# Kernel optimization log

Hardware: AMD Instinct MI355X
Metric: run time of the kernel (lower is better)

The kernel has to match this reference:

```python
import jax, jax.numpy as jnp
import numpy as np

B = 1024        # probe batch
Q = 65536       # queue_size (number of identities in momentum queue)
D = 512         # feat_dim
MARGIN = 0.4
SCALE = 32.0
HARD_NEG = 10   # min(max(int(Q*0.0002), 3), 10)


def setup_inputs() -> dict:
    key = jax.random.key(0)
    k1, k2, k3, k4 = jax.random.split(key, 4)
    p = jax.random.normal(k1, (B, D), dtype=jnp.float32)
    p = p / jnp.linalg.norm(p, axis=1, keepdims=True)
    queue = jax.random.uniform(k2, (2, Q, D), dtype=jnp.float32)
    queue = queue / jnp.linalg.norm(queue, axis=2, keepdims=True)  # F.normalize(queue, dim=2)
    label = jax.random.randint(k3, (B,), 0, Q)
    label = jnp.where(jnp.arange(B) % 4 == 0, -1, label)
    # binary mask buffer marking queue slots whose second copy is active
    mask = (jax.random.uniform(k4, (Q, 1)) < 0.1).astype(jnp.float32)
    return {"p": p, "queue": queue, "mask": mask, "label": label}


def _add_margin_am(cos_theta, label):
    # cos_theta: [B, Q], label: [B] with -1 marking outliers
    pos_mask = label != -1                                  # [B]
    safe_label = jnp.where(pos_mask, label, 0)
    onehot = jax.nn.one_hot(safe_label, cos_theta.shape[1], dtype=cos_theta.dtype)
    # AM-softmax: subtract margin at the ground-truth logit, then scale + CE
    logits = (cos_theta - MARGIN * onehot) * SCALE          # [B, Q]
    log_z = jax.nn.logsumexp(logits, axis=1)                # [B]
    gt = jnp.take_along_axis(cos_theta, safe_label[:, None], axis=1)[:, 0]
    ce = log_z - (gt - MARGIN) * SCALE                      # per-row cross entropy
    n_pos = jnp.sum(pos_mask)
    cls_loss = jnp.where(
        n_pos > 0,
        jnp.sum(jnp.where(pos_mask, ce, 0.0)) / jnp.maximum(n_pos, 1),
        0.0,
    )
    # hard-negative mining over outlier rows: top-k (replaces torch argsort+gather)
    top_vals, _ = jax.lax.top_k(cos_theta, HARD_NEG)        # [B, HARD_NEG]
    hard = jnp.clip(top_vals, 0.0)
    neg_per_row = jnp.mean(hard, axis=1)                    # [B]
    n_neg = jnp.sum(~pos_mask)
    neg_loss = jnp.where(
        n_neg > 0,
        jnp.sum(jnp.where(~pos_mask, neg_per_row, 0.0)) / jnp.maximum(n_neg, 1),
        0.0,
    )
    return cls_loss + neg_loss


def reference(p, queue, mask, label):
    # cos_theta1 = F.linear(p, queue[0])
    cos1 = jnp.einsum('bd,qd->bq', p, queue[0])
    # weight = mask * queue[1] + (1 - mask) * queue[0]  (computed under no_grad in torch)
    weight = mask * queue[1] + (1.0 - mask) * queue[0]
    cos2 = jnp.einsum('bd,qd->bq', p, weight)
    loss = _add_margin_am(cos1, label) + _add_margin_am(cos2, label)
    return loss
```

## Files before the change

### kernel.cpp

```cpp
#include <hip/hip_runtime.h>
#include <stdint.h>

#define B_ 1024
#define Q_ 65536
#define D_ 512
#define MT 128
#define NT 128
#define BK 64
#define NSPLIT 64
#define NCHUNK (Q_ / NSPLIT)
#define NTILES (NCHUNK / NT)
#define KITERS (D_ / BK)

#define SCALE32 32.0f
#define C32 46.16624130844683f

#define WS_ACC  0
#define WS_LSE  4096
#define WS_TOPK (1u * 1024u * 1024u)
#define WS_PBF  (8u * 1024u * 1024u)
#define WS_QBF0 (12u * 1024u * 1024u)
#define WS_WBF  (76u * 1024u * 1024u)

#define SA_OFF 0
#define SB0_OFF 16384
#define SB1_OFF 32768

typedef __attribute__((ext_vector_type(8))) short short8;
typedef __attribute__((ext_vector_type(4))) short short4v;
typedef __attribute__((ext_vector_type(4))) float f32x4;

__device__ __forceinline__ unsigned short f2bf(float x) {
  union { float f; uint32_t u; } v; v.f = x;
  uint32_t r = v.u + 0x7fffu + ((v.u >> 16) & 1u);
  return (unsigned short)(r >> 16);
}

__device__ __forceinline__ float bf2f(short u) {
  union { uint32_t i; float f; } v;
  v.i = ((uint32_t)(unsigned short)u) << 16;
  return v.f;
}

__device__ __forceinline__ void async16(void* lds, const void* g) {
  void* gg = (void*)g;
  __builtin_amdgcn_global_load_lds(
      (__attribute__((address_space(1))) unsigned int*)gg,
      (__attribute__((address_space(3))) unsigned int*)lds,
      16, 0, 0);
}

__device__ __forceinline__ void tkins(float v,
    float& t0, float& t1, float& t2, float& t3, float& t4,
    float& t5, float& t6, float& t7, float& t8, float& t9) {
  if (v > t9) {
    t9 = (v > t8) ? t8 : v;
    t8 = (v > t8) ? ((v > t7) ? t7 : v) : t8;
    t7 = (v > t7) ? ((v > t6) ? t6 : v) : t7;
    t6 = (v > t6) ? ((v > t5) ? t5 : v) : t6;
    t5 = (v > t5) ? ((v > t4) ? t4 : v) : t5;
    t4 = (v > t4) ? ((v > t3) ? t3 : v) : t4;
    t3 = (v > t3) ? ((v > t2) ? t2 : v) : t3;
    t2 = (v > t2) ? ((v > t1) ? t1 : v) : t2;
    t1 = (v > t1) ? ((v > t0) ? t0 : v) : t1;
    t0 = (v > t0) ? v : t0;
  }
}

#define TKA(v, a) tkins((v), a[0], a[1], a[2], a[3], a[4], a[5], a[6], a[7], a[8], a[9])

__global__ void cvt_all(const float* __restrict__ q, const float* __restrict__ p,
                        const float* __restrict__ mask,
                        unsigned short* __restrict__ qbf0,
                        unsigned short* __restrict__ wbf,
                        unsigned short* __restrict__ pbf) {
  const int wv = threadIdx.x >> 6;
  const int lane = threadIdx.x & 63;
  const int b = blockIdx.x;
  if (b < Q_ / 4) {
    const int row = b * 4 + wv;
    const float* q0r = q + (size_t)row * D_ + lane * 8;
    float4 a = ((const float4*)q0r)[0];
    float4 bb = ((const float4*)q0r)[1];
    short8 o;
    o[0] = (short)f2bf(a.x); o[1] = (short)f2bf(a.y);
    o[2] = (short)f2bf(a.z); o[3] = (short)f2bf(a.w);
    o[4] = (short)f2bf(bb.x); o[5] = (short)f2bf(bb.y);
    o[6] = (short)f2bf(bb.z); o[7] = (short)f2bf(bb.w);
    *(short8*)(qbf0 + (size_t)row * D_ + lane * 8) = o;
    float m = mask[row];
    if (m != 0.0f) {
      const float* q1r = q0r + (size_t)Q_ * D_;
      float4 c = ((const float4*)q1r)[0];
      float4 d = ((const float4*)q1r)[1];
      a.x = fmaf(m, c.x - a.x, a.x); a.y = fmaf(m, c.y - a.y, a.y);
      a.z = fmaf(m, c.z - a.z, a.z); a.w = fmaf(m, c.w - a.w, a.w);
      bb.x = fmaf(m, d.x - bb.x, bb.x); bb.y = fmaf(m, d.y - bb.y, bb.y);
      bb.z = fmaf(m, d.z - bb.z, bb.z); bb.w = fmaf(m, d.w - bb.w, bb.w);
      o[0] = (short)f2bf(a.x); o[1] = (short)f2bf(a.y);
      o[2] = (short)f2bf(a.z); o[3] = (short)f2bf(a.w);
      o[4] = (short)f2bf(bb.x); o[5] = (short)f2bf(bb.y);
      o[6] = (short)f2bf(bb.z); o[7] = (short)f2bf(bb.w);
      *(short8*)(wbf + (size_t)row * D_ + lane * 8) = o;
    }
  } else {
    const int row = (b - Q_ / 4) * 4 + wv;
    const float* pr = p + (size_t)row * D_ + lane * 8;
    float4 a = ((const float4*)pr)[0];
    float4 bb = ((const float4*)pr)[1];
    short8 o;
    o[0] = (short)f2bf(a.x); o[1] = (short)f2bf(a.y);
    o[2] = (short)f2bf(a.z); o[3] = (short)f2bf(a.w);
    o[4] = (short)f2bf(bb.x); o[5] = (short)f2bf(bb.y);
    o[6] = (short)f2bf(bb.z); o[7] = (short)f2bf(bb.w);
    *(short8*)(pbf + (size_t)row * D_ + lane * 8) = o;
  }
}

__global__ __launch_bounds__(256, 2) void fused_gemm_partial(
    const unsigned short* __restrict__ pbf,
    const unsigned short* __restrict__ qbf0,
    const unsigned short* __restrict__ wbf,
    const float* __restrict__ maskp,
    const int* __restrict__ label,
    char* __restrict__ ws) {
  __shared__ __align__(16) unsigned char smem[49152];
  __shared__ float maskb[NT];
  __shared__ float zacc[MT][4];
  __shared__ int olist[MT];
  __shared__ int rowmap[MT];
  __shared__ int sh_ocount;

  const int tid = threadIdx.x;
  const int split = blockIdx.x;
  const int mblk = blockIdx.y;
  const int lane = tid & 63;
  const int wv = tid >> 6;
  const int wr = wv >> 1;
  const int wc = wv & 1;
  const int lr = lane & 15;
  const int lg = lane >> 4;

  if (tid == 0) sh_ocount = 0;
  if (tid < MT) {
    rowmap[tid] = -1;
    zacc[tid][0] = 0.0f; zacc[tid][1] = 0.0f;
    zacc[tid][2] = 0.0f; zacc[tid][3] = 0.0f;
  }
  __syncthreads();
  if (tid < MT) {
    if (label[mblk * MT + tid] == -1) {
      int k = atomicAdd(&sh_ocount, 1);
      olist[k] = tid;
    }
  }
  __syncthreads();
  const int noc = sh_ocount;
  if (tid < noc) rowmap[olist[tid]] = tid;
  __syncthreads();
  const int nchunks = (noc + 31) >> 5;

  const int srow = lane >> 3;
  const int sc16 = (lane & 7) ^ srow;
  const size_t g_lane_off = (size_t)srow * D_ + sc16 * 8;

  float T[10];
#pragma unroll
  for (int i = 0; i < 10; ++i) T[i] = -1e30f;

  for (int nt = 0; nt < NTILES; ++nt) {
    const int nbase = split * NCHUNK + nt * NT;
    if (tid < NT) maskb[tid] = maskp[nbase + tid];
    __syncthreads();

    const unsigned short* b1b[4];
#pragma unroll
    for (int t = 0; t < 4; ++t) {
      const int rowl = (wv * 4 + t) * 8 + srow;
      b1b[t] = (maskb[rowl] != 0.0f) ? wbf : qbf0;
    }

    f32x4 acc0[4][4], acc1[4][4];
#pragma unroll
    for (int i = 0; i < 4; ++i)
#pragma unroll
      for (int j = 0; j < 4; ++j) {
        f32x4 z = {0.0f, 0.0f, 0.0f, 0.0f};
        acc0[i][j] = z;
        acc1[i][j] = z;
      }

    for (int kk = 0; kk < KITERS; ++kk) {
      const size_t kcol = (size_t)kk * BK;
#pragma unroll
      for (int t = 0; t < 4; ++t) {
        const int slot = wv * 4 + t;
        const size_t rbase = (size_t)slot * 8;
        async16(smem + SA_OFF + slot * 1024,
                pbf + ((size_t)mblk * MT + rbase) * D_ + kcol + g_lane_off);
        async16(smem + SB0_OFF + slot * 1024,
                qbf0 + ((size_t)nbase + rbase) * D_ + kcol + g_lane_off);
        async16(smem + SB1_OFF + slot * 1024,
                b1b[t] + ((size_t)nbase + rbase) * D_ + kcol + g_lane_off);
      }
      __syncthreads();

#pragma unroll
      for (int s = 0; s < 2; ++s) {
        const int xs = ((s * 4 + lg) ^ (lr & 7)) * 16;
        short8 af[4], bf[4];
#pragma unroll
        for (int i = 0; i < 4; ++i)
          af[i] = *(const short8*)(smem + SA_OFF + (wr * 64 + i * 16 + lr) * 128 + xs);
#pragma unroll
        for (int j = 0; j < 4; ++j)
          bf[j] = *(const short8*)(smem + SB0_OFF + (wc * 64 + j * 16 + lr) * 128 + xs);
#pragma unroll
        for (int i = 0; i < 4; ++i)
#pragma unroll
          for (int j = 0; j < 4; ++j)
            acc0[i][j] = __builtin_amdgcn_mfma_f32_16x16x32_bf16(af[i], bf[j], acc0[i][j], 0, 0, 0);
#pragma unroll
        for (int j = 0; j < 4; ++j)
          bf[j] = *(const short8*)(smem + SB1_OFF + (wc * 64 + j * 16 + lr) * 128 + xs);
#pragma unroll
        for (int i = 0; i < 4; ++i)
#pragma unroll
          for (int j = 0; j < 4; ++j)
            acc1[i][j] = __builtin_amdgcn_mfma_f32_16x16x32_bf16(af[i], bf[j], acc1[i][j], 0, 0, 0);
      }
      __syncthreads();
    }

#pragma unroll
    for (int i = 0; i < 4; ++i)
#pragma unroll
      for (int k = 0; k < 4; ++k) {
        float a0 = 0.0f, a1 = 0.0f;
#pragma unroll
        for (int j = 0; j < 4; ++j) {
          a0 += __builtin_amdgcn_exp2f(fmaf(acc0[i][j][k], C32, -C32));
          a1 += __builtin_amdgcn_exp2f(fmaf(acc1[i][j][k], C32, -C32));
        }
#pragma unroll
        for (int m = 1; m < 16; m <<= 1) {
          a0 += __shfl_xor(a0, m, 64);
          a1 += __shfl_xor(a1, m, 64);
        }
        if (lr == 0) {
          const int r = wr * 64 + i * 16 + lg * 4 + k;
          zacc[r][wc * 2 + 0] += a0;
          zacc[r][wc * 2 + 1] += a1;
        }
      }

    for (int c = 0; c < nchunks; ++c) {
      unsigned short* cp = (unsigned short*)smem;
#pragma unroll
      for (int i = 0; i < 4; ++i)
#pragma unroll
        for (int k = 0; k < 4; ++k) {
          const int r = wr * 64 + i * 16 + lg * 4 + k;
          const int o = rowmap[r];
          const int ol = o - c * 32;
          if (o >= 0 && ol >= 0 && ol < 32) {
#pragma unroll
            for (int j = 0; j < 4; ++j) {
              const int col = wc * 64 + j * 16 + lr;
              cp[ol * 128 + col] = f2bf(acc0[i][j][k]);
              cp[(32 + ol) * 128 + col] = f2bf(acc1[i][j][k]);
            }
          }
        }
      __syncthreads();

      {
        float tl[10];
#pragma unroll
        for (int r = 0; r < 10; ++r) tl[r] = -1e30f;
        const int pair = tid >> 2;
        const int q4 = tid & 3;
        const int orow = pair >> 1, mat = pair & 1;
        const int o = c * 32 + orow;
        if (o < noc) {
          const unsigned short* rp = cp + (mat * 32 + orow) * 128 + q4 * 32;
#pragma unroll
          for (int cc = 0; cc < 8; ++cc) {
            short4v v = *(const short4v*)(rp + cc * 4);
            TKA(bf2f(v.x), tl); TKA(bf2f(v.y), tl);
            TKA(bf2f(v.z), tl); TKA(bf2f(v.w), tl);
          }
          float ot[10];
#pragma unroll
          for (int r = 0; r < 10; ++r) ot[r] = __shfl_xor(tl[r], 1, 64);
#pragma unroll
          for (int r = 0; r < 10; ++r) TKA(ot[r], tl);
#pragma unroll
          for (int r = 0; r < 10; ++r) ot[r] = __shfl_xor(tl[r], 2, 64);
#pragma unroll
          for (int r = 0; r < 10; ++r) TKA(ot[r], tl);
          if (q4 == 0) {
            if (c == 0) {
#pragma unroll
              for (int r = 0; r < 10; ++r) TKA(tl[r], T);
            } else {
              float* slot = (float*)(ws + WS_TOPK) +
                  ((size_t)(mat * B_ + mblk * MT + olist[o]) * NSPLIT + split) * 10;
              if (nt == 0) {
#pragma unroll
                for (int r = 0; r < 10; ++r) slot[r] = tl[r];
              } else {
                float cur[10];
#pragma unroll
                for (int r = 0; r < 10; ++r) cur[r] = slot[r];
#pragma unroll
                for (int r = 0; r < 10; ++r) TKA(tl[r], cur);
#pragma unroll
                for (int r = 0; r < 10; ++r) slot[r] = cur[r];
              }
            }
          }
        }
      }
      __syncthreads();
    }
  }

  if (tid < MT) {
    float2* lseo = (float2*)(ws + WS_LSE);
    lseo[(size_t)(mblk * MT + tid) * NSPLIT + split] =
        make_float2(zacc[tid][0] + zacc[tid][2], zacc[tid][1] + zacc[tid][3]);
  }
  {
    const int pair = tid >> 2;
    const int q4 = tid & 3;
    const int orow = pair >> 1, mat = pair & 1;
    if (q4 == 0 && orow < noc && orow < 32) {
      float* slot = (float*)(ws + WS_TOPK) +
          ((size_t)(mat * B_ + mblk * MT + olist[orow]) * NSPLIT + split) * 10;
#pragma unroll
      for (int r = 0; r < 10; ++r) slot[r] = T[r];
    }
  }
}

__global__ void finalize_rows(
    const float* __restrict__ p, const float* __restrict__ queue,
    const float* __restrict__ maskp, const int* __restrict__ label,
    char* __restrict__ ws, float* __restrict__ out) {
  const int row = blockIdx.x;
  const int l = threadIdx.x >> 6;
  const int lane = threadIdx.x & 63;
  const int lab = label[row];
  float* wsf = (float*)ws;
  int* wsi = (int*)ws;

  if (lab != -1) {
    const float2* lsep = (const float2*)(ws + WS_LSE) + (size_t)row * NSPLIT;
    float2 zz = lsep[lane];
    float z = (l == 0) ? zz.x : zz.y;
#pragma unroll
    for (int o = 1; o < 64; o <<= 1) z += __shfl_xor(z, o, 64);

    const float* prow = p + (size_t)row * D_;
    const float* q0r = queue + (size_t)lab * D_;
    const float* q1r = queue + ((size_t)Q_ + (size_t)lab) * D_;
    int c = lane * 8;
    float4 a0 = *(const float4*)(prow + c);
    float4 a1 = *(const float4*)(prow + c + 4);
    float4 b0 = *(const float4*)(q0r + c);
    float4 b1 = *(const float4*)(q0r + c + 4);
    float d0 = a0.x * b0.x + a0.y * b0.y + a0.z * b0.z + a0.w * b0.w
             + a1.x * b1.x + a1.y * b1.y + a1.z * b1.z + a1.w * b1.w;
    float d1 = 0.0f;
    if (l == 1) {
      float4 c0 = *(const float4*)(q1r + c);
      float4 c1 = *(const float4*)(q1r + c + 4);
      d1 = a0.x * c0.x + a0.y * c0.y + a0.z * c0.z + a0.w * c0.w
         + a1.x * c1.x + a1.y * c1.y + a1.z * c1.z + a1.w * c1.w;
    }
#pragma unroll
    for (int o = 1; o < 64; o <<= 1) {
      d0 += __shfl_xor(d0, o, 64);
      d1 += __shfl_xor(d1, o, 64);
    }
    float gt;
    if (l == 0) gt = d0;
    else { float m = maskp[lab]; gt = fmaf(m, d1 - d0, d0); }

    if (lane == 0) {
      float e1 = __builtin_amdgcn_exp2f(fmaf(gt, C32, -C32));
      float e2 = __builtin_amdgcn_exp2f(fmaf(gt - 0.4f, C32, -C32));
      float Zc = z - e1 + e2;
      float ce = 32.0f + __logf(Zc) - (gt - 0.4f) * SCALE32;
      atomicAdd(&wsf[0], ce);
      if (l == 0) atomicAdd(&wsi[2], 1);
    }
  } else {
    const float* tp = (const float*)(ws + WS_TOPK) +
                      ((size_t)l * B_ + row) * NSPLIT * 10 + (size_t)lane * 10;
    float t0 = tp[0], t1 = tp[1], t2 = tp[2], t3 = tp[3], t4 = tp[4];
    float t5 = tp[5], t6 = tp[6], t7 = tp[7], t8 = tp[8], t9 = tp[9];
    float ssum = 0.0f;
#pragma unroll
    for (int r10 = 0; r10 < 10; ++r10) {
      float v = t0;
      int idx = lane;
#pragma unroll
      for (int o = 1; o < 64; o <<= 1) {
        float ov = __shfl_xor(v, o, 64);
        int oi = __shfl_xor(idx, o, 64);
        bool take = (ov > v) || (ov == v && oi < idx);
        v = take ? ov : v;
        idx = take ? oi : idx;
      }
      ssum += fmaxf(v, 0.0f);
      if (idx == lane) {
        t0 = t1; t1 = t2; t2 = t3; t3 = t4; t4 = t5;
        t5 = t6; t6 = t7; t7 = t8; t8 = t9; t9 = -1e30f;
      }
    }
    if (lane == 0) {
      atomicAdd(&wsf[1], ssum * 0.1f);
      if (l == 0) atomicAdd(&wsi[3], 1);
    }
  }

  __syncthreads();
  if (threadIdx.x == 0) {
    __threadfence();
    int old = atomicAdd(&wsi[4], 1);
    if (old == B_ - 1) {
      float ce = atomicAdd(&wsf[0], 0.0f);
      float ng = atomicAdd(&wsf[1], 0.0f);
      int np = atomicAdd(&wsi[2], 0);
      int nn = atomicAdd(&wsi[3], 0);
      float loss = 0.0f;
      if (np > 0) loss += ce / (float)np;
      if (nn > 0) loss += ng / (float)nn;
      out[0] = loss;
    }
  }
}

extern "C" void kernel_launch(void* const* d_in, const int* in_sizes, int n_in,
                              void* d_out, int out_size, void* d_ws, size_t ws_size,
                              hipStream_t stream) {
  const float* p     = (const float*)d_in[0];
  const float* queue = (const float*)d_in[1];
  const float* maskp = (const float*)d_in[2];
  const int*   label = (const int*)d_in[3];
  float* out = (float*)d_out;
  char* ws = (char*)d_ws;

  unsigned short* pbf  = (unsigned short*)(ws + WS_PBF);
  unsigned short* qbf0 = (unsigned short*)(ws + WS_QBF0);
  unsigned short* wbf  = (unsigned short*)(ws + WS_WBF);

  hipMemsetAsync(ws, 0, 32, stream);

  cvt_all<<<Q_ / 4 + B_ / 4, 256, 0, stream>>>(queue, p, maskp, qbf0, wbf, pbf);

  dim3 g1(NSPLIT, B_ / MT);
  fused_gemm_partial<<<g1, 256, 0, stream>>>(pbf, qbf0, wbf, maskp, label, ws);
  finalize_rows<<<B_, 128, 0, stream>>>(p, queue, maskp, label, ws, out);
}
```

Measured before the change: 594.9 us.

## Compute second GEMM only on masked rows via compacted delta correction

The second matrix product differed from the first only on the roughly 10% of queue rows whose mask is set. So the main GEMM now computes one product, and a separate compacted GEMM over masked rows (their q0 and blended copies) gives a log-sum-exp delta and top-k candidates for the second loss. Top-k for the shared product marks masked columns as -inf and merges them with the compacted results. This roughly halves MFMA work and B-tile traffic, at the cost of an atomic compaction pass, an extra memset, a fixed cap of MMAX masked rows, and a higher split count and occupancy target.

```diff
diff --git a/kernel.cpp b/kernel.cpp
--- a/kernel.cpp
+++ b/kernel.cpp
@@ -7,24 +7,28 @@
 #define MT 128
 #define NT 128
 #define BK 64
-#define NSPLIT 64
+#define NSPLIT 128
 #define NCHUNK (Q_ / NSPLIT)
 #define NTILES (NCHUNK / NT)
 #define KITERS (D_ / BK)
+#define MMAX 8192
+#define MTILES (MMAX / NT)
 
 #define SCALE32 32.0f
 #define C32 46.16624130844683f
 
-#define WS_ACC  0
-#define WS_LSE  4096
-#define WS_TOPK (1u * 1024u * 1024u)
-#define WS_PBF  (8u * 1024u * 1024u)
-#define WS_QBF0 (12u * 1024u * 1024u)
-#define WS_WBF  (76u * 1024u * 1024u)
+#define WS_ZDELTA 64
+#define WS_LSE    8192
+#define WS_TOPK   (1u << 20)
+#define WS_TOPKM  (6u << 20)
+#define WS_PBF    (12u << 20)
+#define WS_QBF0   (16u << 20)
+#define WS_QMC    (80u << 20)
+#define WS_WMC    (88u << 20)
 
 #define SA_OFF 0
-#define SB0_OFF 16384
-#define SB1_OFF 32768
+#define SB_OFF 16384
+#define CPSTRIDE 136
 
 typedef __attribute__((ext_vector_type(8))) short short8;
 typedef __attribute__((ext_vector_type(4))) short short4v;
@@ -66,14 +70,15 @@
     t0 = (v > t0) ? v : t0;
   }
 }
-
 #define TKA(v, a) tkins((v), a[0], a[1], a[2], a[3], a[4], a[5], a[6], a[7], a[8], a[9])
 
 __global__ void cvt_all(const float* __restrict__ q, const float* __restrict__ p,
                         const float* __restrict__ mask,
                         unsigned short* __restrict__ qbf0,
-                        unsigned short* __restrict__ wbf,
-                        unsigned short* __restrict__ pbf) {
+                        unsigned short* __restrict__ pbf,
+                        unsigned short* __restrict__ qmc,
+                        unsigned short* __restrict__ wmc,
+                        int* __restrict__ wsi) {
   const int wv = threadIdx.x >> 6;
   const int lane = threadIdx.x & 63;
   const int b = blockIdx.x;
@@ -90,18 +95,26 @@
     *(short8*)(qbf0 + (size_t)row * D_ + lane * 8) = o;
     float m = mask[row];
     if (m != 0.0f) {
+      int idx = 0;
+      if (lane == 0) idx = atomicAdd(&wsi[5], 1);
+      idx = __shfl(idx, 0, 64);
       const float* q1r = q0r + (size_t)Q_ * D_;
       float4 c = ((const float4*)q1r)[0];
       float4 d = ((const float4*)q1r)[1];
-      a.x = fmaf(m, c.x - a.x, a.x); a.y = fmaf(m, c.y - a.y, a.y);
-      a.z = fmaf(m, c.z - a.z, a.z); a.w = fmaf(m, c.w - a.w, a.w);
-      bb.x = fmaf(m, d.x - bb.x, bb.x); bb.y = fmaf(m, d.y - bb.y, bb.y);
-      bb.z = fmaf(m, d.z - bb.z, bb.z); bb.w = fmaf(m, d.w - bb.w, bb.w);
-      o[0] = (short)f2bf(a.x); o[1] = (short)f2bf(a.y);
-      o[2] = (short)f2bf(a.z); o[3] = (short)f2bf(a.w);
-      o[4] = (short)f2bf(bb.x); o[5] = (short)f2bf(bb.y);
-      o[6] = (short)f2bf(bb.z); o[7] = (short)f2bf(bb.w);
-      *(short8*)(wbf + (size_t)row * D_ + lane * 8) = o;
+      float4 wa, wb;
+      wa.x = fmaf(m, c.x - a.x, a.x); wa.y = fmaf(m, c.y - a.y, a.y);
+      wa.z = fmaf(m, c.z - a.z, a.z); wa.w = fmaf(m, c.w - a.w, a.w);
+      wb.x = fmaf(m, d.x - bb.x, bb.x); wb.y = fmaf(m, d.y - bb.y, bb.y);
+      wb.z = fmaf(m, d.z - bb.z, bb.z); wb.w = fmaf(m, d.w - bb.w, bb.w);
+      short8 o2;
+      o2[0] = (short)f2bf(wa.x); o2[1] = (short)f2bf(wa.y);
+      o2[2] = (short)f2bf(wa.z); o2[3] = (short)f2bf(wa.w);
+      o2[4] = (short)f2bf(wb.x); o2[5] = (short)f2bf(wb.y);
+      o2[6] = (short)f2bf(wb.z); o2[7] = (short)f2bf(wb.w);
+      if (idx < MMAX) {
+        *(short8*)(qmc + (size_t)idx * D_ + lane * 8) = o;
+        *(short8*)(wmc + (size_t)idx * D_ + lane * 8) = o2;
+      }
     }
   } else {
     const int row = (b - Q_ / 4) * 4 + wv;
@@ -117,16 +130,16 @@
   }
 }
 
-__global__ __launch_bounds__(256, 2) void fused_gemm_partial(
+__global__ __launch_bounds__(256, 3) void main_gemm(
     const unsigned short* __restrict__ pbf,
     const unsigned short* __restrict__ qbf0,
-    const unsigned short* __restrict__ wbf,
     const float* __restrict__ maskp,
     const int* __restrict__ label,
     char* __restrict__ ws) {
-  __shared__ __align__(16) unsigned char smem[49152];
+  __shared__ __align__(16) unsigned char smem[32768];
+  __shared__ float Tlds[256][11];
   __shared__ float maskb[NT];
-  __shared__ float zacc[MT][4];
+  __shared__ float zacc[MT][2];
   __shared__ int olist[MT];
   __shared__ int rowmap[MT];
   __shared__ int sh_ocount;
@@ -145,8 +158,9 @@
   if (tid < MT) {
     rowmap[tid] = -1;
     zacc[tid][0] = 0.0f; zacc[tid][1] = 0.0f;
-    zacc[tid][2] = 0.0f; zacc[tid][3] = 0.0f;
-  }
+  }
+#pragma unroll
+  for (int i = 0; i < 10; ++i) Tlds[tid][i] = -1e30f;
   __syncthreads();
   if (tid < MT) {
     if (label[mblk * MT + tid] == -1) {
@@ -164,30 +178,18 @@
   const int sc16 = (lane & 7) ^ srow;
   const size_t g_lane_off = (size_t)srow * D_ + sc16 * 8;
 
-  float T[10];
-#pragma unroll
-  for (int i = 0; i < 10; ++i) T[i] = -1e30f;
-
   for (int nt = 0; nt < NTILES; ++nt) {
     const int nbase = split * NCHUNK + nt * NT;
     if (tid < NT) maskb[tid] = maskp[nbase + tid];
     __syncthreads();
 
-    const unsigned short* b1b[4];
-#pragma unroll
-    for (int t = 0; t < 4; ++t) {
-      const int rowl = (wv * 4 + t) * 8 + srow;
-      b1b[t] = (maskb[rowl] != 0.0f) ? wbf : qbf0;
-    }
-
-    f32x4 acc0[4][4], acc1[4][4];
+    f32x4 acc[4][4];
 #pragma unroll
     for (int i = 0; i < 4; ++i)
 #pragma unroll
       for (int j = 0; j < 4; ++j) {
         f32x4 z = {0.0f, 0.0f, 0.0f, 0.0f};
-        acc0[i][j] = z;
-        acc1[i][j] = z;
+        acc[i][j] = z;
       }
 
     for (int kk = 0; kk < KITERS; ++kk) {
@@ -198,13 +200,10 @@
         const size_t rbase = (size_t)slot * 8;
         async16(smem + SA_OFF + slot * 1024,
                 pbf + ((size_t)mblk * MT + rbase) * D_ + kcol + g_lane_off);
-        async16(smem + SB0_OFF + slot * 1024,
+        async16(smem + SB_OFF + slot * 1024,
                 qbf0 + ((size_t)nbase + rbase) * D_ + kcol + g_lane_off);
-        async16(smem + SB1_OFF + slot * 1024,
-                b1b[t] + ((size_t)nbase + rbase) * D_ + kcol + g_lane_off);
       }
       __syncthreads();
-
 #pragma unroll
       for (int s = 0; s < 2; ++s) {
         const int xs = ((s * 4 + lg) ^ (lr & 7)) * 16;
@@ -214,43 +213,29 @@
           af[i] = *(const short8*)(smem + SA_OFF + (wr * 64 + i * 16 + lr) * 128 + xs);
 #pragma unroll
         for (int j = 0; j < 4; ++j)
-          bf[j] = *(const short8*)(smem + SB0_OFF + (wc * 64 + j * 16 + lr) * 128 + xs);
+          bf[j] = *(const short8*)(smem + SB_OFF + (wc * 64 + j * 16 + lr) * 128 + xs);
 #pragma unroll
         for (int i = 0; i < 4; ++i)
 #pragma unroll
           for (int j = 0; j < 4; ++j)
-            acc0[i][j] = __builtin_amdgcn_mfma_f32_16x16x32_bf16(af[i], bf[j], acc0[i][j], 0, 0, 0);
+            acc[i][j] = __builtin_amdgcn_mfma_f32_16x16x32_bf16(af[i], bf[j], acc[i][j], 0, 0, 0);
+      }
+      __syncthreads();
+    }
+
+#pragma unroll
+    for (int i = 0; i < 4; ++i)
+#pragma unroll
+      for (int k = 0; k < 4; ++k) {
+        float a0 = 0.0f;
 #pragma unroll
         for (int j = 0; j < 4; ++j)
-          bf[j] = *(const short8*)(smem + SB1_OFF + (wc * 64 + j * 16 + lr) * 128 + xs);
-#pragma unroll
-        for (int i = 0; i < 4; ++i)
-#pragma unroll
-          for (int j = 0; j < 4; ++j)
-            acc1[i][j] = __builtin_amdgcn_mfma_f32_16x16x32_bf16(af[i], bf[j], acc1[i][j], 0, 0, 0);
-      }
-      __syncthreads();
-    }
-
-#pragma unroll
-    for (int i = 0; i < 4; ++i)
-#pragma unroll
-      for (int k = 0; k < 4; ++k) {
-        float a0 = 0.0f, a1 = 0.0f;
-#pragma unroll
-        for (int j = 0; j < 4; ++j) {
-          a0 += __builtin_amdgcn_exp2f(fmaf(acc0[i][j][k], C32, -C32));
-          a1 += __builtin_amdgcn_exp2f(fmaf(acc1[i][j][k], C32, -C32));
-        }
-#pragma unroll
-        for (int m = 1; m < 16; m <<= 1) {
-          a0 += __shfl_xor(a0, m, 64);
-          a1 += __shfl_xor(a1, m, 64);
-        }
+          a0 += __builtin_amdgcn_exp2f(fmaf(acc[i][j][k], C32, -C32));
+#pragma unroll
+        for (int m = 1; m < 16; m <<= 1) a0 += __shfl_xor(a0, m, 64);
         if (lr == 0) {
           const int r = wr * 64 + i * 16 + lg * 4 + k;
-          zacc[r][wc * 2 + 0] += a0;
-          zacc[r][wc * 2 + 1] += a1;
+          zacc[r][wc] += a0;
         }
       }
 
@@ -267,80 +252,267 @@
 #pragma unroll
             for (int j = 0; j < 4; ++j) {
               const int col = wc * 64 + j * 16 + lr;
-              cp[ol * 128 + col] = f2bf(acc0[i][j][k]);
-              cp[(32 + ol) * 128 + col] = f2bf(acc1[i][j][k]);
+              unsigned short v = (maskb[col] != 0.0f) ? (unsigned short)0xFF80
+                                                      : f2bf(acc[i][j][k]);
+              cp[ol * CPSTRIDE + col] = v;
             }
           }
         }
       __syncthreads();
 
-      {
-        float tl[10];
-#pragma unroll
-        for (int r = 0; r < 10; ++r) tl[r] = -1e30f;
-        const int pair = tid >> 2;
-        const int q4 = tid & 3;
-        const int orow = pair >> 1, mat = pair & 1;
-        const int o = c * 32 + orow;
+      const int orow = tid >> 3;
+      const int q8 = tid & 7;
+      const int o = c * 32 + orow;
+      if (c == 0) {
         if (o < noc) {
-          const unsigned short* rp = cp + (mat * 32 + orow) * 128 + q4 * 32;
-#pragma unroll
-          for (int cc = 0; cc < 8; ++cc) {
+          float tl[10];
+#pragma unroll
+          for (int r = 0; r < 10; ++r) tl[r] = Tlds[tid][r];
+          const unsigned short* rp = cp + orow * CPSTRIDE + q8 * 16;
+#pragma unroll
+          for (int cc = 0; cc < 4; ++cc) {
             short4v v = *(const short4v*)(rp + cc * 4);
             TKA(bf2f(v.x), tl); TKA(bf2f(v.y), tl);
             TKA(bf2f(v.z), tl); TKA(bf2f(v.w), tl);
           }
-          float ot[10];
-#pragma unroll
-          for (int r = 0; r < 10; ++r) ot[r] = __shfl_xor(tl[r], 1, 64);
-#pragma unroll
-          for (int r = 0; r < 10; ++r) TKA(ot[r], tl);
-#pragma unroll
-          for (int r = 0; r < 10; ++r) ot[r] = __shfl_xor(tl[r], 2, 64);
-#pragma unroll
-          for (int r = 0; r < 10; ++r) TKA(ot[r], tl);
-          if (q4 == 0) {
-            if (c == 0) {
-#pragma unroll
-              for (int r = 0; r < 10; ++r) TKA(tl[r], T);
-            } else {
-              float* slot = (float*)(ws + WS_TOPK) +
-                  ((size_t)(mat * B_ + mblk * MT + olist[o]) * NSPLIT + split) * 10;
-              if (nt == 0) {
-#pragma unroll
-                for (int r = 0; r < 10; ++r) slot[r] = tl[r];
-              } else {
-                float cur[10];
-#pragma unroll
-                for (int r = 0; r < 10; ++r) cur[r] = slot[r];
-#pragma unroll
-                for (int r = 0; r < 10; ++r) TKA(tl[r], cur);
-#pragma unroll
-                for (int r = 0; r < 10; ++r) slot[r] = cur[r];
-              }
-            }
+#pragma unroll
+          for (int r = 0; r < 10; ++r) Tlds[tid][r] = tl[r];
+        }
+      } else {
+        float tl[10];
+#pragma unroll
+        for (int r = 0; r < 10; ++r) tl[r] = -1e30f;
+        if (o < noc) {
+          const unsigned short* rp = cp + orow * CPSTRIDE + q8 * 16;
+#pragma unroll
+          for (int cc = 0; cc < 4; ++cc) {
+            short4v v = *(const short4v*)(rp + cc * 4);
+            TKA(bf2f(v.x), tl); TKA(bf2f(v.y), tl);
+            TKA(bf2f(v.z), tl); TKA(bf2f(v.w), tl);
           }
         }
+        float ot[10];
+#pragma unroll
+        for (int m = 1; m < 8; m <<= 1) {
+#pragma unroll
+          for (int r = 0; r < 10; ++r) ot[r] = __shfl_xor(tl[r], m, 64);
+#pragma unroll
+          for (int r = 0; r < 10; ++r) TKA(ot[r], tl);
+        }
+        if (q8 == 0 && o < noc) {
+          float* slot = (float*)(ws + WS_TOPK) +
+              ((size_t)(mblk * MT + olist[o]) * NSPLIT + split) * 10;
+          if (nt == 0) {
+#pragma unroll
+            for (int r = 0; r < 10; ++r) slot[r] = tl[r];
+          } else {
+            float cur[10];
+#pragma unroll
+            for (int r = 0; r < 10; ++r) cur[r] = slot[r];
+#pragma unroll
+            for (int r = 0; r < 10; ++r) TKA(tl[r], cur);
+#pragma unroll
+            for (int r = 0; r < 10; ++r) slot[r] = cur[r];
+          }
+        }
       }
       __syncthreads();
     }
   }
 
   if (tid < MT) {
-    float2* lseo = (float2*)(ws + WS_LSE);
-    lseo[(size_t)(mblk * MT + tid) * NSPLIT + split] =
-        make_float2(zacc[tid][0] + zacc[tid][2], zacc[tid][1] + zacc[tid][3]);
+    ((float*)(ws + WS_LSE))[(size_t)(mblk * MT + tid) * NSPLIT + split] =
+        zacc[tid][0] + zacc[tid][1];
   }
   {
-    const int pair = tid >> 2;
-    const int q4 = tid & 3;
-    const int orow = pair >> 1, mat = pair & 1;
-    if (q4 == 0 && orow < noc && orow < 32) {
+    const int orow = tid >> 3;
+    const int q8 = tid & 7;
+    float tl[10], ot[10];
+#pragma unroll
+    for (int r = 0; r < 10; ++r) tl[r] = Tlds[tid][r];
+#pragma unroll
+    for (int m = 1; m < 8; m <<= 1) {
+#pragma unroll
+      for (int r = 0; r < 10; ++r) ot[r] = __shfl_xor(tl[r], m, 64);
+#pragma unroll
+      for (int r = 0; r < 10; ++r) TKA(ot[r], tl);
+    }
+    if (q8 == 0 && orow < noc) {
       float* slot = (float*)(ws + WS_TOPK) +
-          ((size_t)(mat * B_ + mblk * MT + olist[orow]) * NSPLIT + split) * 10;
-#pragma unroll
-      for (int r = 0; r < 10; ++r) slot[r] = T[r];
-    }
+          ((size_t)(mblk * MT + olist[orow]) * NSPLIT + split) * 10;
+#pragma unroll
+      for (int r = 0; r < 10; ++r) slot[r] = tl[r];
+    }
+  }
+}
+
+__global__ __launch_bounds__(256, 3) void masked_gemm(
+    const unsigned short* __restrict__ pbf,
+    const unsigned short* __restrict__ qmc,
+    const unsigned short* __restrict__ wmc,
+    const int* __restrict__ label,
+    char* __restrict__ ws) {
+  __shared__ __align__(16) unsigned char smem[32768];
+  __shared__ float zacc[MT][2];
+  __shared__ int olist[MT];
+  __shared__ int rowmap[MT];
+  __shared__ int sh_ocount;
+
+  const int tid = threadIdx.x;
+  const int tile = blockIdx.x;
+  const int mblk = blockIdx.y;
+  const int half = blockIdx.z;
+  const int lane = tid & 63;
+  const int wv = tid >> 6;
+  const int wr = wv >> 1;
+  const int wc = wv & 1;
+  const int lr = lane & 15;
+  const int lg = lane >> 4;
+  const int* wsi = (const int*)ws;
+
+  if (tid == 0) sh_ocount = 0;
+  if (tid < MT) {
+    rowmap[tid] = -1;
+    zacc[tid][0] = 0.0f; zacc[tid][1] = 0.0f;
+  }
+  __syncthreads();
+  if (tid < MT) {
+    if (label[mblk * MT + tid] == -1) {
+      int k = atomicAdd(&sh_ocount, 1);
+      olist[k] = tid;
+    }
+  }
+  __syncthreads();
+  const int noc = sh_ocount;
+  if (tid < noc) rowmap[olist[tid]] = tid;
+  __syncthreads();
+  const int nchunks = (noc + 31) >> 5;
+  const int mcnt = wsi[5];
+
+  if (tile * NT >= mcnt) {
+    if (tid < noc) {
+      float* slot = (float*)(ws + WS_TOPKM) +
+          (((size_t)half * B_ + mblk * MT + olist[tid]) * MTILES + tile) * 10;
+#pragma unroll
+      for (int r = 0; r < 10; ++r) slot[r] = -1e30f;
+    }
+    return;
+  }
+
+  const unsigned short* bsrc = half ? wmc : qmc;
+  const int nbase = tile * NT;
+  const int srow = lane >> 3;
+  const int sc16 = (lane & 7) ^ srow;
+  const size_t g_lane_off = (size_t)srow * D_ + sc16 * 8;
+
+  f32x4 acc[4][4];
+#pragma unroll
+  for (int i = 0; i < 4; ++i)
+#pragma unroll
+    for (int j = 0; j < 4; ++j) {
+      f32x4 z = {0.0f, 0.0f, 0.0f, 0.0f};
+      acc[i][j] = z;
+    }
+
+  for (int kk = 0; kk < KITERS; ++kk) {
+    const size_t kcol = (size_t)kk * BK;
+#pragma unroll
+    for (int t = 0; t < 4; ++t) {
+      const int slot = wv * 4 + t;
+      const size_t rbase = (size_t)slot * 8;
+      async16(smem + SA_OFF + slot * 1024,
+              pbf + ((size_t)mblk * MT + rbase) * D_ + kcol + g_lane_off);
+      async16(smem + SB_OFF + slot * 1024,
+              bsrc + ((size_t)nbase + rbase) * D_ + kcol + g_lane_off);
+    }
+    __syncthreads();
+#pragma unroll
+    for (int s = 0; s < 2; ++s) {
+      const int xs = ((s * 4 + lg) ^ (lr & 7)) * 16;
+      short8 af[4], bf[4];
+#pragma unroll
+      for (int i = 0; i < 4; ++i)
+        af[i] = *(const short8*)(smem + SA_OFF + (wr * 64 + i * 16 + lr) * 128 + xs);
+#pragma unroll
+      for (int j = 0; j < 4; ++j)
+        bf[j] = *(const short8*)(smem + SB_OFF + (wc * 64 + j * 16 + lr) * 128 + xs);
+#pragma unroll
+      for (int i = 0; i < 4; ++i)
+#pragma unroll
+        for (int j = 0; j < 4; ++j)
+          acc[i][j] = __builtin_amdgcn_mfma_f32_16x16x32_bf16(af[i], bf[j], acc[i][j], 0, 0, 0);
+    }
+    __syncthreads();
+  }
+
+#pragma unroll
+  for (int i = 0; i < 4; ++i)
+#pragma unroll
+    for (int k = 0; k < 4; ++k) {
+      float a0 = 0.0f;
+#pragma unroll
+      for (int j = 0; j < 4; ++j)
+        a0 += __builtin_amdgcn_exp2f(fmaf(acc[i][j][k], C32, -C32));
+#pragma unroll
+      for (int m = 1; m < 16; m <<= 1) a0 += __shfl_xor(a0, m, 64);
+      if (lr == 0) {
+        const int r = wr * 64 + i * 16 + lg * 4 + k;
+        zacc[r][wc] += a0;
+      }
+    }
+  __syncthreads();
+  if (tid < MT) {
+    float z = zacc[tid][0] + zacc[tid][1];
+    atomicAdd((float*)(ws + WS_ZDELTA) + (mblk * MT + tid), half ? z : -z);
+  }
+
+  for (int c = 0; c < nchunks; ++c) {
+    unsigned short* cp = (unsigned short*)smem;
+#pragma unroll
+    for (int i = 0; i < 4; ++i)
+#pragma unroll
+      for (int k = 0; k < 4; ++k) {
+        const int r = wr * 64 + i * 16 + lg * 4 + k;
+        const int o = rowmap[r];
+        const int ol = o - c * 32;
+        if (o >= 0 && ol >= 0 && ol < 32) {
+#pragma unroll
+          for (int j = 0; j < 4; ++j) {
+            const int col = wc * 64 + j * 16 + lr;
+            cp[ol * CPSTRIDE + col] = f2bf(acc[i][j][k]);
+          }
+        }
+      }
+    __syncthreads();
+    const int orow = tid >> 3;
+    const int q8 = tid & 7;
+    const int o = c * 32 + orow;
+    float tl[10], ot[10];
+#pragma unroll
+    for (int r = 0; r < 10; ++r) tl[r] = -1e30f;
+    if (o < noc) {
+      const unsigned short* rp = cp + orow * CPSTRIDE + q8 * 16;
+#pragma unroll
+      for (int cc = 0; cc < 4; ++cc) {
+        short4v v = *(const short4v*)(rp + cc * 4);
+        TKA(bf2f(v.x), tl); TKA(bf2f(v.y), tl);
+        TKA(bf2f(v.z), tl); TKA(bf2f(v.w), tl);
+      }
+    }
+#pragma unroll
+    for (int m = 1; m < 8; m <<= 1) {
+#pragma unroll
+      for (int r = 0; r < 10; ++r) ot[r] = __shfl_xor(tl[r], m, 64);
+#pragma unroll
+      for (int r = 0; r < 10; ++r) TKA(ot[r], tl);
+    }
+    if (q8 == 0 && o < noc) {
+      float* slot = (float*)(ws + WS_TOPKM) +
+          (((size_t)half * B_ + mblk * MT + olist[o]) * MTILES + tile) * 10;
+#pragma unroll
+      for (int r = 0; r < 10; ++r) slot[r] = tl[r];
+    }
+    __syncthreads();
   }
 }
 
@@ -356,11 +528,11 @@
   int* wsi = (int*)ws;
 
   if (lab != -1) {
-    const float2* lsep = (const float2*)(ws + WS_LSE) + (size_t)row * NSPLIT;
-    float2 zz = lsep[lane];
-    float z = (l == 0) ? zz.x : zz.y;
+    const float* lsep = (const float*)(ws + WS_LSE) + (size_t)row * NSPLIT;
+    float z = lsep[lane] + lsep[lane + 64];
 #pragma unroll
     for (int o = 1; o < 64; o <<= 1) z += __shfl_xor(z, o, 64);
+    if (l == 1) z += ((const float*)(ws + WS_ZDELTA))[row];
 
     const float* prow = p + (size_t)row * D_;
     const float* q0r = queue + (size_t)lab * D_;
@@ -397,10 +569,18 @@
       if (l == 0) atomicAdd(&wsi[2], 1);
     }
   } else {
-    const float* tp = (const float*)(ws + WS_TOPK) +
-                      ((size_t)l * B_ + row) * NSPLIT * 10 + (size_t)lane * 10;
-    float t0 = tp[0], t1 = tp[1], t2 = tp[2], t3 = tp[3], t4 = tp[4];
-    float t5 = tp[5], t6 = tp[6], t7 = tp[7], t8 = tp[8], t9 = tp[9];
+    const float* Lm1 = (const float*)(ws + WS_TOPK) + ((size_t)row * NSPLIT + lane) * 10;
+    const float* Lm2 = (const float*)(ws + WS_TOPK) + ((size_t)row * NSPLIT + 64 + lane) * 10;
+    const float* Lk  = (const float*)(ws + WS_TOPKM) +
+                       (((size_t)l * B_ + row) * MTILES + lane) * 10;
+    float t0 = Lm1[0], t1 = Lm1[1], t2 = Lm1[2], t3 = Lm1[3], t4 = Lm1[4];
+    float t5 = Lm1[5], t6 = Lm1[6], t7 = Lm1[7], t8 = Lm1[8], t9 = Lm1[9];
+#pragma unroll
+    for (int i = 0; i < 10; ++i)
+      tkins(Lm2[i], t0, t1, t2, t3, t4, t5, t6, t7, t8, t9);
+#pragma unroll
+    for (int i = 0; i < 10; ++i)
+      tkins(Lk[i], t0, t1, t2, t3, t4, t5, t6, t7, t8, t9);
     float ssum = 0.0f;
 #pragma unroll
     for (int r10 = 0; r10 < 10; ++r10) {
@@ -455,13 +635,16 @@
 
   unsigned short* pbf  = (unsigned short*)(ws + WS_PBF);
   unsigned short* qbf0 = (unsigned short*)(ws + WS_QBF0);
-  unsigned short* wbf  = (unsigned short*)(ws + WS_WBF);
-
-  hipMemsetAsync(ws, 0, 32, stream);
-
-  cvt_all<<<Q_ / 4 + B_ / 4, 256, 0, stream>>>(queue, p, maskp, qbf0, wbf, pbf);
-
-  dim3 g1(NSPLIT, B_ / MT);
-  fused_gemm_partial<<<g1, 256, 0, stream>>>(pbf, qbf0, wbf, maskp, label, ws);
+  unsigned short* qmc  = (unsigned short*)(ws + WS_QMC);
+  unsigned short* wmc  = (unsigned short*)(ws + WS_WMC);
+
+  hipMemsetAsync(ws, 0, WS_ZDELTA + B_ * 4, stream);
+  hipMemsetAsync(ws + WS_QMC, 0, 2u * MMAX * D_ * 2u, stream);
+
+  cvt_all<<<Q_ / 4 + B_ / 4, 256, 0, stream>>>(queue, p, maskp, qbf0, pbf,
+                                               qmc, wmc, (int*)ws);
+
+  masked_gemm<<<dim3(MTILES, B_ / MT, 2), 256, 0, stream>>>(pbf, qmc, wmc, label, ws);
+  main_gemm<<<dim3(NSPLIT, B_ / MT), 256, 0, stream>>>(pbf, qbf0, maskp, label, ws);
   finalize_rows<<<B_, 128, 0, stream>>>(p, queue, maskp, label, ws, out);
 }
```

New measurement: 652.4 us. +9.7%, slower.
